# Kernel tuning notes

Hardware: AMD Instinct MI355X
Metric: run time of the kernel (lower is better)

The kernel has to match this reference:

```python
import jax, jax.numpy as jnp
import numpy as np

DIM = 768
HEADS = 12
HEAD_DIM = DIM // HEADS
SCALE = HEAD_DIM ** -0.5


def setup_inputs() -> dict:
    key = jax.random.key(0)
    ks = jax.random.split(key, 5)
    x = jax.random.normal(ks[0], (2, 4096, DIM), dtype=jnp.float32)
    # torch nn.Linear params: weight [out, in], bias [out]
    qkv_w = jax.random.normal(ks[1], (3 * DIM, DIM), dtype=jnp.float32) * (DIM ** -0.5)
    qkv_b = jax.random.normal(ks[2], (3 * DIM,), dtype=jnp.float32) * 0.02
    proj_w = jax.random.normal(ks[3], (DIM, DIM), dtype=jnp.float32) * (DIM ** -0.5)
    proj_b = jax.random.normal(ks[4], (DIM,), dtype=jnp.float32) * 0.02
    return {"x": x, "qkv_w": qkv_w, "qkv_b": qkv_b, "proj_w": proj_w, "proj_b": proj_b}


def reference(x, qkv_w, qkv_b, proj_w, proj_b):
    b, n, c = x.shape
    qkv = x @ qkv_w.T + qkv_b                      # [b, n, 3c]
    qkv = qkv.reshape(b, n, 3, HEADS, HEAD_DIM)
    qkv = jnp.transpose(qkv, (2, 0, 3, 1, 4))      # [3, b, h, n, d]
    q, k, v = qkv[0], qkv[1], qkv[2]
    attn = jax.nn.softmax(jnp.einsum('bhqd,bhkd->bhqk', q, k) * SCALE, axis=-1)
    out = jnp.einsum('bhqk,bhkd->bhqd', attn, v)   # [b, h, n, d]
    out = jnp.transpose(out, (0, 2, 1, 3)).reshape(b, n, c)
    return out @ proj_w.T + proj_b
```

## Files before the change

kernel.cpp:

```cpp
#include <hip/hip_runtime.h>
#include <stdint.h>

#define SEQ   4096
#define NDIM  768
#define HD    64
#define NH    12
#define NBH   24
#define MTOT  8192

#define LSTR 40
#define PSTR 72

typedef short s8v __attribute__((ext_vector_type(8)));
typedef float f4v __attribute__((ext_vector_type(4)));
typedef float f16x __attribute__((ext_vector_type(16)));
typedef unsigned short u16;
typedef u16 u16x4 __attribute__((ext_vector_type(4)));
typedef uint32_t u32x4v __attribute__((ext_vector_type(4)));
typedef int i32x2 __attribute__((ext_vector_type(2)));

#define C1 0.18033688011112042f

__device__ __forceinline__ u16 f2bf(float f) {
  union { float f; uint32_t u; } cv; cv.f = f;
  const uint32_t u = cv.u;
  return (u16)((u + 0x7fffu + ((u >> 16) & 1u)) >> 16);
}
__device__ __forceinline__ float ex2(float x) { return __builtin_amdgcn_exp2f(x); }

__device__ __forceinline__ uint32_t cvtpk_bf16(float lo, float hi) {
  uint32_t r;
  asm("v_cvt_pk_bf16_f32 %0, %1, %2" : "=v"(r) : "v"(lo), "v"(hi));
  return r;
}
__device__ __forceinline__ void pl32swap(uint32_t& a, uint32_t& b) {
  i32x2 r = __builtin_amdgcn_permlane32_swap((int)a, (int)b, false, false);
  a = (uint32_t)r.x; b = (uint32_t)r.y;
}

__global__ __launch_bounds__(256) void cvt3_kernel(
    const float* __restrict__ a, u16* __restrict__ da, int na4,
    const float* __restrict__ b, u16* __restrict__ db, int nb4,
    const float* __restrict__ c, u16* __restrict__ dc, int nc4) {
  int i = blockIdx.x * 256 + threadIdx.x;
  const float* s; u16* d;
  if (i < na4)             { s = a; d = da; }
  else if (i < na4 + nb4)  { s = b; d = db; i -= na4; }
  else if (i < na4 + nb4 + nc4) { s = c; d = dc; i -= na4 + nb4; }
  else return;
  const float4 f = ((const float4*)s)[i];
  u16x4 r;
  r[0] = f2bf(f.x); r[1] = f2bf(f.y); r[2] = f2bf(f.z); r[3] = f2bf(f.w);
  ((u16x4*)d)[i] = r;
}

__global__ __launch_bounds__(256) void gemm_qkv(const u16* __restrict__ A,
    const u16* __restrict__ B, const float* __restrict__ bias,
    u16* __restrict__ qg, u16* __restrict__ kg, u16* __restrict__ vtg) {
  __shared__ __align__(16) u16 at[128 * LSTR];
  __shared__ __align__(16) u16 bt[128 * LSTR];
  const int tid  = threadIdx.x;
  const int lane = tid & 63;
  const int w    = tid >> 6;
  const int quad = lane >> 4;
  const int col  = lane & 15;
  const int m0 = blockIdx.y * 128;
  const int n0 = blockIdx.x * 128;
  const int srow = tid >> 2;
  const int sch  = (tid & 3) * 8;
  const int wm = (w >> 1) * 64;
  const int wn = (w & 1) * 64;

  const f4v fz = {0.f, 0.f, 0.f, 0.f};
  f4v acc[4][4];
#pragma unroll
  for (int i = 0; i < 4; i++)
#pragma unroll
    for (int j = 0; j < 4; j++) acc[i][j] = fz;

  const u16* ap0 = A + (size_t)(m0 + srow) * NDIM + sch;
  const u16* ap1 = A + (size_t)(m0 + 64 + srow) * NDIM + sch;
  const u16* bp0 = B + (size_t)(n0 + srow) * NDIM + sch;
  const u16* bp1 = B + (size_t)(n0 + 64 + srow) * NDIM + sch;

  for (int k0 = 0; k0 < NDIM; k0 += 32) {
    const s8v va0 = *(const s8v*)(ap0 + k0);
    const s8v va1 = *(const s8v*)(ap1 + k0);
    const s8v vb0 = *(const s8v*)(bp0 + k0);
    const s8v vb1 = *(const s8v*)(bp1 + k0);
    __syncthreads();
    *(s8v*)(at + srow * LSTR + sch) = va0;
    *(s8v*)(at + (64 + srow) * LSTR + sch) = va1;
    *(s8v*)(bt + srow * LSTR + sch) = vb0;
    *(s8v*)(bt + (64 + srow) * LSTR + sch) = vb1;
    __syncthreads();
    s8v af[4], bf[4];
#pragma unroll
    for (int i = 0; i < 4; i++)
      af[i] = *(const s8v*)(at + (wm + i * 16 + col) * LSTR + quad * 8);
#pragma unroll
    for (int j = 0; j < 4; j++)
      bf[j] = *(const s8v*)(bt + (wn + j * 16 + col) * LSTR + quad * 8);
#pragma unroll
    for (int i = 0; i < 4; i++)
#pragma unroll
      for (int j = 0; j < 4; j++)
        acc[i][j] = __builtin_amdgcn_mfma_f32_16x16x32_bf16(af[i], bf[j], acc[i][j], 0, 0, 0);
  }

  const int wmg = m0 + wm;
  const int wng = n0 + wn;
  const int s = n0 / NDIM;
#pragma unroll
  for (int j = 0; j < 4; j++) {
    const int c = wng + j * 16 + col;
    const float bv = bias[c];
    const int r = c - s * NDIM;
    const int h = r >> 6;
    const int d = r & 63;
#pragma unroll
    for (int i = 0; i < 4; i++) {
      const int mb = wmg + i * 16 + quad * 4;
      const int bb = mb >> 12;
      const int n  = mb & 4095;
      const size_t hb = (size_t)(bb * NH + h);
      const f4v v = acc[i][j];
      if (s == 2) {
        u16x4 pk;
#pragma unroll
        for (int rg = 0; rg < 4; rg++) pk[rg] = f2bf(v[rg] + bv);
        *(u16x4*)(vtg + (hb * HD + d) * SEQ + n) = pk;
      } else if (s == 0) {
#pragma unroll
        for (int rg = 0; rg < 4; rg++)
          qg[(hb * SEQ + (size_t)(n + rg)) * HD + d] = f2bf((v[rg] + bv) * C1);
      } else {
#pragma unroll
        for (int rg = 0; rg < 4; rg++)
          kg[(hb * SEQ + (size_t)(n + rg)) * HD + d] = f2bf(v[rg] + bv);
      }
    }
  }
}

__global__ __launch_bounds__(256, 3) void attn_kernel(const u16* __restrict__ qg,
    const u16* __restrict__ kg, const u16* __restrict__ vtg, u16* __restrict__ og) {
  __shared__ __align__(16) u16 kls[2][64 * PSTR];
  __shared__ __align__(16) u16 vls[2][64 * PSTR];
  __shared__ float lws[4][32];

  const int tid  = threadIdx.x;
  const int lane = tid & 63;
  const int w    = tid >> 6;
  const int hi   = lane >> 5;
  const int c    = lane & 31;
  const int blk = blockIdx.x;
  const int bh  = blk % NBH;
  const int q0  = (blk / NBH) * 128;
  const size_t gbase = (size_t)bh * (SEQ * HD);
  const int wq = w * 32;

  s8v qf[4];
#pragma unroll
  for (int s = 0; s < 4; s++)
    qf[s] = *(const s8v*)(qg + gbase + (size_t)(q0 + wq + c) * HD + s * 16 + hi * 8);

  f16x o0, o1;
#pragma unroll
  for (int e = 0; e < 16; e++) { o0[e] = 0.f; o1[e] = 0.f; }
  float l0 = 0.f, l1 = 0.f, l2 = 0.f, l3 = 0.f;

  const int srow8 = tid >> 3;
  const int sch8  = (tid & 7) * 8;
  const u16* kp = kg  + gbase + (size_t)srow8 * HD  + sch8;
  const u16* vp = vtg + gbase + (size_t)srow8 * SEQ;

  s8v kr0 = *(const s8v*)(kp);
  s8v kr1 = *(const s8v*)(kp + (size_t)32 * HD);
  s8v vr0 = *(const s8v*)(vp + sch8);
  s8v vr1 = *(const s8v*)(vp + (size_t)32 * SEQ + sch8);
  *(s8v*)(kls[0] + srow8 * PSTR + sch8) = kr0;
  *(s8v*)(kls[0] + (32 + srow8) * PSTR + sch8) = kr1;
  *(s8v*)(vls[0] + srow8 * PSTR + sch8) = vr0;
  *(s8v*)(vls[0] + (32 + srow8) * PSTR + sch8) = vr1;

  for (int kb = 0; kb < SEQ; kb += 64) {
    const int cur = (kb >> 6) & 1;
    const u16* kt_ = kls[cur];
    const u16* vt_ = vls[cur];
    __syncthreads();

    if (kb + 64 < SEQ) {
      kr0 = *(const s8v*)(kp + (size_t)(kb + 64) * HD);
      kr1 = *(const s8v*)(kp + (size_t)(kb + 96) * HD);
      vr0 = *(const s8v*)(vp + kb + 64 + sch8);
      vr1 = *(const s8v*)(vp + (size_t)32 * SEQ + kb + 64 + sch8);
    }

    f16x st0, st1;
#pragma unroll
    for (int e = 0; e < 16; e++) { st0[e] = 0.f; st1[e] = 0.f; }
#pragma unroll
    for (int s = 0; s < 4; s++) {
      const s8v k0 = *(const s8v*)(kt_ + c * PSTR + s * 16 + hi * 8);
      const s8v k1 = *(const s8v*)(kt_ + (32 + c) * PSTR + s * 16 + hi * 8);
      st0 = __builtin_amdgcn_mfma_f32_32x32x16_bf16(k0, qf[s], st0, 0, 0, 0);
      st1 = __builtin_amdgcn_mfma_f32_32x32x16_bf16(k1, qf[s], st1, 0, 0, 0);
    }

    s8v pa0, pa1, pa2, pa3;
    {
      float p[16];
#pragma unroll
      for (int e = 0; e < 16; e++) p[e] = ex2(st0[e]);
      l0 += p[0] + p[4] + p[8]  + p[12];
      l1 += p[1] + p[5] + p[9]  + p[13];
      l2 += p[2] + p[6] + p[10] + p[14];
      l3 += p[3] + p[7] + p[11] + p[15];
      uint32_t k0 = cvtpk_bf16(p[0],  p[1]);
      uint32_t k1 = cvtpk_bf16(p[2],  p[3]);
      uint32_t k2 = cvtpk_bf16(p[4],  p[5]);
      uint32_t k3 = cvtpk_bf16(p[6],  p[7]);
      uint32_t k4 = cvtpk_bf16(p[8],  p[9]);
      uint32_t k5 = cvtpk_bf16(p[10], p[11]);
      uint32_t k6 = cvtpk_bf16(p[12], p[13]);
      uint32_t k7 = cvtpk_bf16(p[14], p[15]);
      pl32swap(k0, k2); pl32swap(k1, k3);
      pl32swap(k4, k6); pl32swap(k5, k7);
      u32x4v wA = {k0, k1, k2, k3};
      u32x4v wB = {k4, k5, k6, k7};
      pa0 = __builtin_bit_cast(s8v, wA);
      pa1 = __builtin_bit_cast(s8v, wB);
    }
    {
      float p[16];
#pragma unroll
      for (int e = 0; e < 16; e++) p[e] = ex2(st1[e]);
      l0 += p[0] + p[4] + p[8]  + p[12];
      l1 += p[1] + p[5] + p[9]  + p[13];
      l2 += p[2] + p[6] + p[10] + p[14];
      l3 += p[3] + p[7] + p[11] + p[15];
      uint32_t k0 = cvtpk_bf16(p[0],  p[1]);
      uint32_t k1 = cvtpk_bf16(p[2],  p[3]);
      uint32_t k2 = cvtpk_bf16(p[4],  p[5]);
      uint32_t k3 = cvtpk_bf16(p[6],  p[7]);
      uint32_t k4 = cvtpk_bf16(p[8],  p[9]);
      uint32_t k5 = cvtpk_bf16(p[10], p[11]);
      uint32_t k6 = cvtpk_bf16(p[12], p[13]);
      uint32_t k7 = cvtpk_bf16(p[14], p[15]);
      pl32swap(k0, k2); pl32swap(k1, k3);
      pl32swap(k4, k6); pl32swap(k5, k7);
      u32x4v wA = {k0, k1, k2, k3};
      u32x4v wB = {k4, k5, k6, k7};
      pa2 = __builtin_bit_cast(s8v, wA);
      pa3 = __builtin_bit_cast(s8v, wB);
    }

#pragma unroll
    for (int ks = 0; ks < 4; ks++) {
      const s8v pv = ks == 0 ? pa0 : ks == 1 ? pa1 : ks == 2 ? pa2 : pa3;
      const s8v v0 = *(const s8v*)(vt_ + c * PSTR + ks * 16 + hi * 8);
      const s8v v1 = *(const s8v*)(vt_ + (32 + c) * PSTR + ks * 16 + hi * 8);
      o0 = __builtin_amdgcn_mfma_f32_32x32x16_bf16(pv, v0, o0, 0, 0, 0);
      o1 = __builtin_amdgcn_mfma_f32_32x32x16_bf16(pv, v1, o1, 0, 0, 0);
    }

    if (kb + 64 < SEQ) {
      u16* kn = (u16*)kls[cur ^ 1];
      u16* vn = (u16*)vls[cur ^ 1];
      *(s8v*)(kn + srow8 * PSTR + sch8) = kr0;
      *(s8v*)(kn + (32 + srow8) * PSTR + sch8) = kr1;
      *(s8v*)(vn + srow8 * PSTR + sch8) = vr0;
      *(s8v*)(vn + (32 + srow8) * PSTR + sch8) = vr1;
    }
  }

  float lt = l0 + l1 + l2 + l3;
  lt += __shfl_xor(lt, 32);
  const float inv = 1.0f / lt;
  if (hi == 0) lws[w][c] = inv;

  const int b = bh / NH;
  const int h = bh % NH;
  u16* obase = og + (size_t)(b * SEQ + q0 + wq) * NDIM + h * HD + c;
#pragma unroll
  for (int r = 0; r < 16; r++) {
    const int row = (r & 3) + 8 * (r >> 2) + 4 * hi;
    const float invr = lws[w][row];
    u16* rp = obase + (size_t)row * NDIM;
    rp[0]  = f2bf(o0[r] * invr);
    rp[32] = f2bf(o1[r] * invr);
  }
}

__global__ __launch_bounds__(256) void gemm_proj(const u16* __restrict__ A,
    const u16* __restrict__ B, const float* __restrict__ bias, float* __restrict__ out) {
  __shared__ __align__(16) u16 at[128 * LSTR];
  __shared__ __align__(16) u16 bt[128 * LSTR];
  const int tid  = threadIdx.x;
  const int lane = tid & 63;
  const int w    = tid >> 6;
  const int quad = lane >> 4;
  const int col  = lane & 15;
  const int m0 = blockIdx.y * 128;
  const int n0 = blockIdx.x * 128;
  const int srow = tid >> 2;
  const int sch  = (tid & 3) * 8;
  const int wm = (w >> 1) * 64;
  const int wn = (w & 1) * 64;

  const f4v fz = {0.f, 0.f, 0.f, 0.f};
  f4v acc[4][4];
#pragma unroll
  for (int i = 0; i < 4; i++)
#pragma unroll
    for (int j = 0; j < 4; j++) acc[i][j] = fz;

  const u16* ap0 = A + (size_t)(m0 + srow) * NDIM + sch;
  const u16* ap1 = A + (size_t)(m0 + 64 + srow) * NDIM + sch;
  const u16* bp0 = B + (size_t)(n0 + srow) * NDIM + sch;
  const u16* bp1 = B + (size_t)(n0 + 64 + srow) * NDIM + sch;

  for (int k0 = 0; k0 < NDIM; k0 += 32) {
    const s8v va0 = *(const s8v*)(ap0 + k0);
    const s8v va1 = *(const s8v*)(ap1 + k0);
    const s8v vb0 = *(const s8v*)(bp0 + k0);
    const s8v vb1 = *(const s8v*)(bp1 + k0);
    __syncthreads();
    *(s8v*)(at + srow * LSTR + sch) = va0;
    *(s8v*)(at + (64 + srow) * LSTR + sch) = va1;
    *(s8v*)(bt + srow * LSTR + sch) = vb0;
    *(s8v*)(bt + (64 + srow) * LSTR + sch) = vb1;
    __syncthreads();
    s8v af[4], bf[4];
#pragma unroll
    for (int i = 0; i < 4; i++)
      af[i] = *(const s8v*)(at + (wm + i * 16 + col) * LSTR + quad * 8);
#pragma unroll
    for (int j = 0; j < 4; j++)
      bf[j] = *(const s8v*)(bt + (wn + j * 16 + col) * LSTR + quad * 8);
#pragma unroll
    for (int i = 0; i < 4; i++)
#pragma unroll
      for (int j = 0; j < 4; j++)
        acc[i][j] = __builtin_amdgcn_mfma_f32_16x16x32_bf16(af[i], bf[j], acc[i][j], 0, 0, 0);
  }

  const int wmg = m0 + wm;
  const int wng = n0 + wn;
#pragma unroll
  for (int j = 0; j < 4; j++) {
    const int c = wng + j * 16 + col;
    const float bv = bias[c];
#pragma unroll
    for (int i = 0; i < 4; i++) {
#pragma unroll
      for (int rg = 0; rg < 4; rg++)
        out[(size_t)(wmg + i * 16 + quad * 4 + rg) * NDIM + c] = acc[i][j][rg] + bv;
    }
  }
}

extern "C" void kernel_launch(void* const* d_in, const int* in_sizes, int n_in,
                              void* d_out, int out_size, void* d_ws, size_t ws_size,
                              hipStream_t stream) {
  const float* x      = (const float*)d_in[0];
  const float* qkv_w  = (const float*)d_in[1];
  const float* qkv_b  = (const float*)d_in[2];
  const float* proj_w = (const float*)d_in[3];
  const float* proj_b = (const float*)d_in[4];
  float* out = (float*)d_out;

  u16* ws   = (u16*)d_ws;
  u16* x_bf = ws;
  u16* wq   = x_bf + (size_t)MTOT * NDIM;
  u16* wp   = wq + (size_t)3 * NDIM * NDIM;
  u16* q_bf = wp + (size_t)NDIM * NDIM;
  u16* k_bf = q_bf + (size_t)NBH * SEQ * HD;
  u16* vt   = k_bf + (size_t)NBH * SEQ * HD;
  u16* a_bf = vt + (size_t)NBH * SEQ * HD;

  const int nx = MTOT * NDIM / 4, nw1 = 3 * NDIM * NDIM / 4, nw2 = NDIM * NDIM / 4;
  const int ntot = nx + nw1 + nw2;
  cvt3_kernel<<<(ntot + 255) / 256, 256, 0, stream>>>(x, x_bf, nx, qkv_w, wq, nw1,
                                                      proj_w, wp, nw2);

  gemm_qkv<<<dim3(18, 64), 256, 0, stream>>>(x_bf, wq, qkv_b, q_bf, k_bf, vt);
  attn_kernel<<<768, 256, 0, stream>>>(q_bf, k_bf, vt, a_bf);
  gemm_proj<<<dim3(6, 64), 256, 0, stream>>>(a_bf, wp, proj_b, out);
}
```

Before: 285.2 us.

## Fuse x bf16 conversion into QKV GEMM, interleave PV MFMAs, shrink proj tiles

The QKV GEMM now reads the fp32 activations directly and packs them to bf16 while staging into shared memory, so the separate x conversion pass and its extra global round-trip go away. The attention loop splits the PV MFMAs into two halves placed between the softmax blocks and the next-tile LDS stores, with s_setprio raised around the MFMA groups to overlap matrix and vector work. The projection GEMM uses 64-row M tiles, doubling the block count to better fill the GPU. The cost is that each QKV block now reads fp32 x from global, which doubles A-side load bytes per block compared with the bf16 copy.

```diff
diff --git a/kernel.cpp b/kernel.cpp
--- a/kernel.cpp
+++ b/kernel.cpp
@@ -38,15 +38,13 @@
   a = (uint32_t)r.x; b = (uint32_t)r.y;
 }
 
-__global__ __launch_bounds__(256) void cvt3_kernel(
+__global__ __launch_bounds__(256) void cvt2_kernel(
     const float* __restrict__ a, u16* __restrict__ da, int na4,
-    const float* __restrict__ b, u16* __restrict__ db, int nb4,
-    const float* __restrict__ c, u16* __restrict__ dc, int nc4) {
+    const float* __restrict__ b, u16* __restrict__ db, int nb4) {
   int i = blockIdx.x * 256 + threadIdx.x;
   const float* s; u16* d;
   if (i < na4)             { s = a; d = da; }
   else if (i < na4 + nb4)  { s = b; d = db; i -= na4; }
-  else if (i < na4 + nb4 + nc4) { s = c; d = dc; i -= na4 + nb4; }
   else return;
   const float4 f = ((const float4*)s)[i];
   u16x4 r;
@@ -54,7 +52,7 @@
   ((u16x4*)d)[i] = r;
 }
 
-__global__ __launch_bounds__(256) void gemm_qkv(const u16* __restrict__ A,
+__global__ __launch_bounds__(256) void gemm_qkv(const float* __restrict__ A,
     const u16* __restrict__ B, const float* __restrict__ bias,
     u16* __restrict__ qg, u16* __restrict__ kg, u16* __restrict__ vtg) {
   __shared__ __align__(16) u16 at[128 * LSTR];
@@ -78,19 +76,30 @@
 #pragma unroll
     for (int j = 0; j < 4; j++) acc[i][j] = fz;
 
-  const u16* ap0 = A + (size_t)(m0 + srow) * NDIM + sch;
-  const u16* ap1 = A + (size_t)(m0 + 64 + srow) * NDIM + sch;
+  const float* ap0 = A + (size_t)(m0 + srow) * NDIM + sch;
+  const float* ap1 = A + (size_t)(m0 + 64 + srow) * NDIM + sch;
   const u16* bp0 = B + (size_t)(n0 + srow) * NDIM + sch;
   const u16* bp1 = B + (size_t)(n0 + 64 + srow) * NDIM + sch;
 
   for (int k0 = 0; k0 < NDIM; k0 += 32) {
-    const s8v va0 = *(const s8v*)(ap0 + k0);
-    const s8v va1 = *(const s8v*)(ap1 + k0);
+    const float4 fa00 = *(const float4*)(ap0 + k0);
+    const float4 fa01 = *(const float4*)(ap0 + k0 + 4);
+    const float4 fa10 = *(const float4*)(ap1 + k0);
+    const float4 fa11 = *(const float4*)(ap1 + k0 + 4);
     const s8v vb0 = *(const s8v*)(bp0 + k0);
     const s8v vb1 = *(const s8v*)(bp1 + k0);
+    u32x4v pk0, pk1;
+    pk0[0] = cvtpk_bf16(fa00.x, fa00.y);
+    pk0[1] = cvtpk_bf16(fa00.z, fa00.w);
+    pk0[2] = cvtpk_bf16(fa01.x, fa01.y);
+    pk0[3] = cvtpk_bf16(fa01.z, fa01.w);
+    pk1[0] = cvtpk_bf16(fa10.x, fa10.y);
+    pk1[1] = cvtpk_bf16(fa10.z, fa10.w);
+    pk1[2] = cvtpk_bf16(fa11.x, fa11.y);
+    pk1[3] = cvtpk_bf16(fa11.z, fa11.w);
     __syncthreads();
-    *(s8v*)(at + srow * LSTR + sch) = va0;
-    *(s8v*)(at + (64 + srow) * LSTR + sch) = va1;
+    *(u32x4v*)(at + srow * LSTR + sch) = pk0;
+    *(u32x4v*)(at + (64 + srow) * LSTR + sch) = pk1;
     *(s8v*)(bt + srow * LSTR + sch) = vb0;
     *(s8v*)(bt + (64 + srow) * LSTR + sch) = vb1;
     __syncthreads();
@@ -200,6 +209,7 @@
     f16x st0, st1;
 #pragma unroll
     for (int e = 0; e < 16; e++) { st0[e] = 0.f; st1[e] = 0.f; }
+    __builtin_amdgcn_s_setprio(1);
 #pragma unroll
     for (int s = 0; s < 4; s++) {
       const s8v k0 = *(const s8v*)(kt_ + c * PSTR + s * 16 + hi * 8);
@@ -207,6 +217,7 @@
       st0 = __builtin_amdgcn_mfma_f32_32x32x16_bf16(k0, qf[s], st0, 0, 0, 0);
       st1 = __builtin_amdgcn_mfma_f32_32x32x16_bf16(k1, qf[s], st1, 0, 0, 0);
     }
+    __builtin_amdgcn_s_setprio(0);
 
     s8v pa0, pa1, pa2, pa3;
     {
@@ -232,6 +243,20 @@
       pa0 = __builtin_bit_cast(s8v, wA);
       pa1 = __builtin_bit_cast(s8v, wB);
     }
+
+    __builtin_amdgcn_s_setprio(1);
+    {
+      const s8v v00 = *(const s8v*)(vt_ + c * PSTR + hi * 8);
+      const s8v v01 = *(const s8v*)(vt_ + (32 + c) * PSTR + hi * 8);
+      const s8v v10 = *(const s8v*)(vt_ + c * PSTR + 16 + hi * 8);
+      const s8v v11 = *(const s8v*)(vt_ + (32 + c) * PSTR + 16 + hi * 8);
+      o0 = __builtin_amdgcn_mfma_f32_32x32x16_bf16(pa0, v00, o0, 0, 0, 0);
+      o1 = __builtin_amdgcn_mfma_f32_32x32x16_bf16(pa0, v01, o1, 0, 0, 0);
+      o0 = __builtin_amdgcn_mfma_f32_32x32x16_bf16(pa1, v10, o0, 0, 0, 0);
+      o1 = __builtin_amdgcn_mfma_f32_32x32x16_bf16(pa1, v11, o1, 0, 0, 0);
+    }
+    __builtin_amdgcn_s_setprio(0);
+
     {
       float p[16];
 #pragma unroll
@@ -256,15 +281,6 @@
       pa3 = __builtin_bit_cast(s8v, wB);
     }
 
-#pragma unroll
-    for (int ks = 0; ks < 4; ks++) {
-      const s8v pv = ks == 0 ? pa0 : ks == 1 ? pa1 : ks == 2 ? pa2 : pa3;
-      const s8v v0 = *(const s8v*)(vt_ + c * PSTR + ks * 16 + hi * 8);
-      const s8v v1 = *(const s8v*)(vt_ + (32 + c) * PSTR + ks * 16 + hi * 8);
-      o0 = __builtin_amdgcn_mfma_f32_32x32x16_bf16(pv, v0, o0, 0, 0, 0);
-      o1 = __builtin_amdgcn_mfma_f32_32x32x16_bf16(pv, v1, o1, 0, 0, 0);
-    }
-
     if (kb + 64 < SEQ) {
       u16* kn = (u16*)kls[cur ^ 1];
       u16* vn = (u16*)vls[cur ^ 1];
@@ -273,6 +289,19 @@
       *(s8v*)(vn + srow8 * PSTR + sch8) = vr0;
       *(s8v*)(vn + (32 + srow8) * PSTR + sch8) = vr1;
     }
+
+    __builtin_amdgcn_s_setprio(1);
+    {
+      const s8v v20 = *(const s8v*)(vt_ + c * PSTR + 32 + hi * 8);
+      const s8v v21 = *(const s8v*)(vt_ + (32 + c) * PSTR + 32 + hi * 8);
+      const s8v v30 = *(const s8v*)(vt_ + c * PSTR + 48 + hi * 8);
+      const s8v v31 = *(const s8v*)(vt_ + (32 + c) * PSTR + 48 + hi * 8);
+      o0 = __builtin_amdgcn_mfma_f32_32x32x16_bf16(pa2, v20, o0, 0, 0, 0);
+      o1 = __builtin_amdgcn_mfma_f32_32x32x16_bf16(pa2, v21, o1, 0, 0, 0);
+      o0 = __builtin_amdgcn_mfma_f32_32x32x16_bf16(pa3, v30, o0, 0, 0, 0);
+      o1 = __builtin_amdgcn_mfma_f32_32x32x16_bf16(pa3, v31, o1, 0, 0, 0);
+    }
+    __builtin_amdgcn_s_setprio(0);
   }
 
   float lt = l0 + l1 + l2 + l3;
@@ -295,52 +324,49 @@
 
 __global__ __launch_bounds__(256) void gemm_proj(const u16* __restrict__ A,
     const u16* __restrict__ B, const float* __restrict__ bias, float* __restrict__ out) {
-  __shared__ __align__(16) u16 at[128 * LSTR];
+  __shared__ __align__(16) u16 at[64 * LSTR];
   __shared__ __align__(16) u16 bt[128 * LSTR];
   const int tid  = threadIdx.x;
   const int lane = tid & 63;
   const int w    = tid >> 6;
   const int quad = lane >> 4;
   const int col  = lane & 15;
-  const int m0 = blockIdx.y * 128;
+  const int m0 = blockIdx.y * 64;
   const int n0 = blockIdx.x * 128;
   const int srow = tid >> 2;
   const int sch  = (tid & 3) * 8;
-  const int wm = (w >> 1) * 64;
+  const int wm = (w >> 1) * 32;
   const int wn = (w & 1) * 64;
 
   const f4v fz = {0.f, 0.f, 0.f, 0.f};
-  f4v acc[4][4];
-#pragma unroll
-  for (int i = 0; i < 4; i++)
+  f4v acc[2][4];
+#pragma unroll
+  for (int i = 0; i < 2; i++)
 #pragma unroll
     for (int j = 0; j < 4; j++) acc[i][j] = fz;
 
   const u16* ap0 = A + (size_t)(m0 + srow) * NDIM + sch;
-  const u16* ap1 = A + (size_t)(m0 + 64 + srow) * NDIM + sch;
   const u16* bp0 = B + (size_t)(n0 + srow) * NDIM + sch;
   const u16* bp1 = B + (size_t)(n0 + 64 + srow) * NDIM + sch;
 
   for (int k0 = 0; k0 < NDIM; k0 += 32) {
     const s8v va0 = *(const s8v*)(ap0 + k0);
-    const s8v va1 = *(const s8v*)(ap1 + k0);
     const s8v vb0 = *(const s8v*)(bp0 + k0);
     const s8v vb1 = *(const s8v*)(bp1 + k0);
     __syncthreads();
     *(s8v*)(at + srow * LSTR + sch) = va0;
-    *(s8v*)(at + (64 + srow) * LSTR + sch) = va1;
     *(s8v*)(bt + srow * LSTR + sch) = vb0;
     *(s8v*)(bt + (64 + srow) * LSTR + sch) = vb1;
     __syncthreads();
-    s8v af[4], bf[4];
-#pragma unroll
-    for (int i = 0; i < 4; i++)
+    s8v af[2], bf[4];
+#pragma unroll
+    for (int i = 0; i < 2; i++)
       af[i] = *(const s8v*)(at + (wm + i * 16 + col) * LSTR + quad * 8);
 #pragma unroll
     for (int j = 0; j < 4; j++)
       bf[j] = *(const s8v*)(bt + (wn + j * 16 + col) * LSTR + quad * 8);
 #pragma unroll
-    for (int i = 0; i < 4; i++)
+    for (int i = 0; i < 2; i++)
 #pragma unroll
       for (int j = 0; j < 4; j++)
         acc[i][j] = __builtin_amdgcn_mfma_f32_16x16x32_bf16(af[i], bf[j], acc[i][j], 0, 0, 0);
@@ -353,7 +379,7 @@
     const int c = wng + j * 16 + col;
     const float bv = bias[c];
 #pragma unroll
-    for (int i = 0; i < 4; i++) {
+    for (int i = 0; i < 2; i++) {
 #pragma unroll
       for (int rg = 0; rg < 4; rg++)
         out[(size_t)(wmg + i * 16 + quad * 4 + rg) * NDIM + c] = acc[i][j][rg] + bv;
@@ -380,12 +406,11 @@
   u16* vt   = k_bf + (size_t)NBH * SEQ * HD;
   u16* a_bf = vt + (size_t)NBH * SEQ * HD;
 
-  const int nx = MTOT * NDIM / 4, nw1 = 3 * NDIM * NDIM / 4, nw2 = NDIM * NDIM / 4;
-  const int ntot = nx + nw1 + nw2;
-  cvt3_kernel<<<(ntot + 255) / 256, 256, 0, stream>>>(x, x_bf, nx, qkv_w, wq, nw1,
-                                                      proj_w, wp, nw2);
-
-  gemm_qkv<<<dim3(18, 64), 256, 0, stream>>>(x_bf, wq, qkv_b, q_bf, k_bf, vt);
+  const int nw1 = 3 * NDIM * NDIM / 4, nw2 = NDIM * NDIM / 4;
+  const int ntot = nw1 + nw2;
+  cvt2_kernel<<<(ntot + 255) / 256, 256, 0, stream>>>(qkv_w, wq, nw1, proj_w, wp, nw2);
+
+  gemm_qkv<<<dim3(18, 64), 256, 0, stream>>>(x, wq, qkv_b, q_bf, k_bf, vt);
   attn_kernel<<<768, 256, 0, stream>>>(q_bf, k_bf, vt, a_bf);
-  gemm_proj<<<dim3(6, 64), 256, 0, stream>>>(a_bf, wp, proj_b, out);
-}
+  gemm_proj<<<dim3(6, 128), 256, 0, stream>>>(a_bf, wp, proj_b, out);
+}
```

Measured after the change: 292.0 us. 1.02x slower.
